# Kernel optimization log

Measured on AMD Instinct MI355X. Metric: run time of the kernel, lower is better.

## Reference

```python
import jax, jax.numpy as jnp
import numpy as np

N_DRUG, N_MICROBE = 1500, 1572
N = N_DRUG + N_MICROBE          # 3072 nodes
F_IN = 1546                     # raw feature dim (fc1: 1546 -> 256)
D0 = 256                        # GCN input dim after fc1
H1 = H2 = 128                   # GCN hidden dims (H1 + H2 = 256)
B = 16384                       # number of (left,right) query pairs


def _sym_norm(A):
    # D^{-1/2} A D^{-1/2} (no self loops), zeros kept for isolated nodes
    deg = A.sum(axis=1)
    d = jnp.where(deg > 0, jax.lax.rsqrt(deg), 0.0)
    return A * d[:, None] * d[None, :]


def _compute_inf(adj, L):
    # dl.compute_inf: L-hop influence = L-th power of sym-normalized adjacency
    An = _sym_norm(adj)
    M = An
    for _ in range(L - 1):
        M = M @ An
    return M


def _gcn_norm(W):
    # GCNConv normalization: add self loops (weight 1), sym-normalize by weighted degree
    Ahat = W + jnp.eye(W.shape[0], dtype=W.dtype)
    deg = Ahat.sum(axis=1)
    d = jnp.where(deg > 0, jax.lax.rsqrt(deg), 0.0)
    return Ahat * d[:, None] * d[None, :]


def _glorot(key, shape):
    return jax.random.normal(key, shape, dtype=jnp.float32) / np.sqrt(shape[0])


def setup_inputs() -> dict:
    key = jax.random.key(0)
    ks = jax.random.split(key, 24)
    u = jax.random.uniform(ks[0], (N, N), dtype=jnp.float32)
    w = jax.random.uniform(ks[1], (N, N), dtype=jnp.float32)
    adj = jnp.where(u < 0.01, w, 0.0)
    adj = jnp.maximum(adj, adj.T)
    X = jax.random.normal(ks[2], (N, F_IN), dtype=jnp.float32)
    left = jax.random.randint(ks[3], (B,), 0, N)
    right = jax.random.randint(ks[4], (B,), 0, N)
    return dict(
        left=left, right=right, X=X, adj=adj, threshold=jnp.float32(1e-4),
        W_fc1=_glorot(ks[5], (F_IN, D0)), b_fc1=jnp.zeros((D0,), jnp.float32),
        Wg1=_glorot(ks[6], (D0, H1)), bg1=jnp.zeros((H1,), jnp.float32),
        Wg2=_glorot(ks[7], (H1, H2)), bg2=jnp.zeros((H2,), jnp.float32),
        Wg3=_glorot(ks[8], (D0, H1)), bg3=jnp.zeros((H1,), jnp.float32),
        Wg4=_glorot(ks[9], (H1, H2)), bg4=jnp.zeros((H2,), jnp.float32),
        Wg5=_glorot(ks[10], (D0, H1)), bg5=jnp.zeros((H1,), jnp.float32),
        Wg6=_glorot(ks[11], (H1, H2)), bg6=jnp.zeros((H2,), jnp.float32),
        cnn_k=jax.random.normal(ks[12], (1, 3, 3, 3), dtype=jnp.float32) * 0.1,
        cnn_b=jnp.zeros((1,), jnp.float32),
        W_a=_glorot(ks[13], (2 * (H1 + H2), 64)), b_a=jnp.zeros((64,), jnp.float32),
        W_b=_glorot(ks[14], (64, 2)), b_b=jnp.zeros((2,), jnp.float32),
    )


def reference(left, right, X, adj, threshold,
              W_fc1, b_fc1, Wg1, bg1, Wg2, bg2, Wg3, bg3, Wg4, bg4,
              Wg5, bg5, Wg6, bg6, cnn_k, cnn_b, W_a, b_a, W_b, b_b):
    X0 = jax.nn.relu(X @ W_fc1 + b_fc1)  # fc1: [N, 1546] -> [N, 256]

    def branch(mask_src, Wa, ba, Wb, bb):
        # dynamically thresholded edges carry the ORIGINAL adj weights
        Wadj = jnp.where(mask_src > threshold, adj, 0.0)
        An = _gcn_norm(Wadj)                       # [N, N]
        e1 = jax.nn.relu(An @ (X0 @ Wa) + ba)      # GCNConv 1
        e2 = jax.nn.relu(An @ (e1 @ Wb) + bb)      # GCNConv 2
        return jnp.concatenate([e1, e2], axis=1)   # [N, 256]

    emb_l2 = branch(_compute_inf(adj, 2), Wg1, bg1, Wg2, bg2)
    emb_l1 = branch(_compute_inf(adj, 1), Wg3, bg3, Wg4, bg4)
    emb_l0 = branch(adj, Wg5, bg5, Wg6, bg6)

    emb = jnp.stack([emb_l0, emb_l1, emb_l2], axis=0)[None]  # [1, 3, N, 256]
    conv = jax.lax.conv_general_dilated(
        emb, cnn_k, window_strides=(1, 1), padding=[(2, 2), (2, 2)],
        rhs_dilation=(2, 2), dimension_numbers=('NCHW', 'OIHW', 'NCHW'))
    emb_all = conv[0, 0] + cnn_b[0]                # [N, 256]

    pair = jnp.concatenate([emb_all[left], emb_all[right]], axis=1)  # [B, 512]
    h = jax.nn.relu(pair @ W_a + b_a)              # dropout is identity at eval
    logits = h @ W_b + b_b                         # [B, 2]
    return logits, emb_all
```

## Files before the change

kernel.cpp:

```cpp
#include <hip/hip_runtime.h>

#define NN 3072
#define FIN 1546
#define KP 1568
#define MAXR 192
#define KSPLIT 7
#define KSLICE 224

#define XS4_BLOCKS (NN * KP / 1024)
#define WSPLIT_BLOCKS (256 * KP / 256)
#define WG_BLOCKS 704
#define CSR_BLOCKS (NN / 4)

typedef __attribute__((ext_vector_type(8))) __bf16 bf16x8;
typedef __attribute__((ext_vector_type(4))) __bf16 bf16x4;
typedef __attribute__((ext_vector_type(4))) float f32x4;

__global__ __launch_bounds__(256) void prep_k(const float* __restrict__ adj,
                                              int* __restrict__ cols, float* __restrict__ vals,
                                              int* __restrict__ cnt, float* __restrict__ dvec,
                                              const float* __restrict__ X,
                                              __bf16* __restrict__ Xh, __bf16* __restrict__ Xl,
                                              const float* __restrict__ W,
                                              __bf16* __restrict__ WhT, __bf16* __restrict__ WlT,
                                              const float* __restrict__ Wga0,
                                              const float* __restrict__ Wga1,
                                              const float* __restrict__ Wga2,
                                              const float* __restrict__ Wgb0,
                                              const float* __restrict__ Wgb1,
                                              const float* __restrict__ Wgb2,
                                              const float* __restrict__ Wa,
                                              __bf16* __restrict__ WgaTh, __bf16* __restrict__ WgaTl,
                                              __bf16* __restrict__ WgbTh, __bf16* __restrict__ WgbTl,
                                              __bf16* __restrict__ WaTh, __bf16* __restrict__ WaTl) {
    int bid = blockIdx.x;
    if (bid < XS4_BLOCKS) {
        int e = (bid * 256 + threadIdx.x) * 4;
        int i = e / KP, c = e - i * KP;
        const float* xr = X + (size_t)i * FIN + c;
        float x0 = (c + 0 < FIN) ? xr[0] : 0.f;
        float x1 = (c + 1 < FIN) ? xr[1] : 0.f;
        float x2 = (c + 2 < FIN) ? xr[2] : 0.f;
        float x3 = (c + 3 < FIN) ? xr[3] : 0.f;
        __bf16 h0 = (__bf16)x0, h1 = (__bf16)x1, h2 = (__bf16)x2, h3 = (__bf16)x3;
        bf16x4 hv = {h0, h1, h2, h3};
        bf16x4 lv = {(__bf16)(x0 - (float)h0), (__bf16)(x1 - (float)h1),
                     (__bf16)(x2 - (float)h2), (__bf16)(x3 - (float)h3)};
        *(bf16x4*)(Xh + e) = hv;
        *(bf16x4*)(Xl + e) = lv;
        return;
    }
    bid -= XS4_BLOCKS;
    if (bid < WSPLIT_BLOCKS) {
        int idx = bid * 256 + threadIdx.x;
        int c = idx / KP, k = idx - c * KP;
        float x = (k < FIN) ? W[(size_t)k * 256 + c] : 0.f;
        __bf16 h = (__bf16)x;
        WhT[idx] = h;
        WlT[idx] = (__bf16)(x - (float)h);
        return;
    }
    bid -= WSPLIT_BLOCKS;
    if (bid < WG_BLOCKS) {
        int idx = bid * 256 + threadIdx.x;
        float x;
        __bf16 *oh, *ol;
        int off;
        if (idx < 98304) {
            int b = idx >> 15, r = idx & 32767;
            int c = r >> 8, k = r & 255;
            const float* Wp = (b == 0) ? Wga0 : (b == 1) ? Wga1 : Wga2;
            x = Wp[k * 128 + c];
            oh = WgaTh; ol = WgaTl; off = idx;
        } else if (idx < 98304 + 49152) {
            int j = idx - 98304;
            int b = j >> 14, r = j & 16383;
            int c = r >> 7, k = r & 127;
            const float* Wp = (b == 0) ? Wgb0 : (b == 1) ? Wgb1 : Wgb2;
            x = Wp[k * 128 + c];
            oh = WgbTh; ol = WgbTl; off = j;
        } else {
            int j = idx - 147456;
            int c = j >> 8, k = j & 255;
            x = (c < 64) ? Wa[(size_t)k * 64 + c] : Wa[(size_t)(256 + k) * 64 + (c - 64)];
            oh = WaTh; ol = WaTl; off = j;
        }
        __bf16 h = (__bf16)x;
        oh[off] = h;
        ol[off] = (__bf16)(x - (float)h);
        return;
    }
    bid -= WG_BLOCKS;
    int i = bid * 4 + (threadIdx.x >> 6);
    int lane = threadIdx.x & 63;
    const float* row = adj + (size_t)i * NN;
    unsigned long long below = (1ull << lane) - 1ull;
    float s = 0.f; int count = 0;
    int base = i * MAXR;
    for (int c0 = 0; c0 < NN; c0 += 256) {
        float4 a4 = *(const float4*)(row + c0 + lane * 4);
        float a[4] = {a4.x, a4.y, a4.z, a4.w};
        s += a[0] + a[1] + a[2] + a[3];
        unsigned long long bal[4];
        #pragma unroll
        for (int u = 0; u < 4; u++) bal[u] = __ballot(a[u] != 0.f);
        int before = 0;
        #pragma unroll
        for (int u = 0; u < 4; u++) before += __popcll(bal[u] & below);
        int local = 0;
        #pragma unroll
        for (int u = 0; u < 4; u++) {
            if (a[u] != 0.f) {
                int pos = count + before + local;
                if (pos < MAXR) { cols[base + pos] = c0 + lane * 4 + u; vals[base + pos] = a[u]; }
                local++;
            }
        }
        int tot = 0;
        #pragma unroll
        for (int u = 0; u < 4; u++) tot += __popcll(bal[u]);
        count += tot;
    }
    for (int off = 32; off; off >>= 1) s += __shfl_xor(s, off);
    if (lane == 0) {
        cnt[i] = count < MAXR ? count : MAXR;
        dvec[i] = (s > 0.f) ? 1.0f / sqrtf(s) : 0.f;
    }
}

__global__ __launch_bounds__(256) void fc1m_k(const __bf16* __restrict__ Xh,
                                              const __bf16* __restrict__ Xl,
                                              const __bf16* __restrict__ WhT,
                                              const __bf16* __restrict__ WlT,
                                              float* __restrict__ Cpart) {
    int tid = threadIdx.x;
    int w = tid >> 6, lane = tid & 63;
    int m = lane & 15, q = lane >> 4;
    int i0 = blockIdx.x * 64, c0 = blockIdx.y * 64;
    int z = blockIdx.z;
    int k0 = z * KSLICE;
    int rowA = i0 + w * 16 + m;
    const __bf16* xh = Xh + (size_t)rowA * KP + k0 + q * 8;
    const __bf16* xl = Xl + (size_t)rowA * KP + k0 + q * 8;
    const __bf16* bh0 = WhT + (size_t)(c0 + m) * KP + k0 + q * 8;
    const __bf16* bl0 = WlT + (size_t)(c0 + m) * KP + k0 + q * 8;

    f32x4 acc[4];
    #pragma unroll
    for (int ct = 0; ct < 4; ct++)
        #pragma unroll
        for (int r = 0; r < 4; r++) acc[ct][r] = 0.f;

    for (int ks = 0; ks < KSLICE; ks += 32) {
        bf16x8 ah = *(const bf16x8*)(xh + ks);
        bf16x8 al = *(const bf16x8*)(xl + ks);
        #pragma unroll
        for (int ct = 0; ct < 4; ct++) {
            bf16x8 bh = *(const bf16x8*)(bh0 + (size_t)ct * 16 * KP + ks);
            bf16x8 bl = *(const bf16x8*)(bl0 + (size_t)ct * 16 * KP + ks);
            acc[ct] = __builtin_amdgcn_mfma_f32_16x16x32_bf16(ah, bh, acc[ct], 0, 0, 0);
            acc[ct] = __builtin_amdgcn_mfma_f32_16x16x32_bf16(ah, bl, acc[ct], 0, 0, 0);
            acc[ct] = __builtin_amdgcn_mfma_f32_16x16x32_bf16(al, bh, acc[ct], 0, 0, 0);
        }
    }
    float* outp = Cpart + (size_t)z * NN * 256;
    int rowBase = i0 + w * 16 + q * 4;
    #pragma unroll
    for (int ct = 0; ct < 4; ct++) {
        int col = c0 + ct * 16 + m;
        #pragma unroll
        for (int r = 0; r < 4; r++)
            outp[(size_t)(rowBase + r) * 256 + col] = acc[ct][r];
    }
}

__global__ __launch_bounds__(256) void maskall_k(const int* __restrict__ cols,
                                                 const float* __restrict__ vals,
                                                 const int* __restrict__ cnt,
                                                 const float* __restrict__ dvec,
                                                 const float* __restrict__ thrp,
                                                 int* __restrict__ mcols,
                                                 float* __restrict__ mvals,
                                                 int* __restrict__ mcnt,
                                                 float* __restrict__ db,
                                                 const float* __restrict__ Cpart,
                                                 const float* __restrict__ bias,
                                                 __bf16* __restrict__ X0h,
                                                 __bf16* __restrict__ X0l) {
    __shared__ float ds[NN];
    __shared__ int lcols[MAXR];
    __shared__ float lvals[MAXR];
    __shared__ int lcnt;
    __shared__ float osum;
    int i = blockIdx.x, tid = threadIdx.x, mode = blockIdx.y;

    if (mode == 3) {
        if (tid < 64) {
            int idx4 = i * 64 + tid;
            int c4 = tid << 2;
            float4 s = ((const float4*)Cpart)[idx4];
            #pragma unroll
            for (int z = 1; z < KSPLIT; z++) {
                float4 t = ((const float4*)(Cpart + (size_t)z * NN * 256))[idx4];
                s.x += t.x; s.y += t.y; s.z += t.z; s.w += t.w;
            }
            float4 b = *(const float4*)&bias[c4];
            s.x = fmaxf(s.x + b.x, 0.f); s.y = fmaxf(s.y + b.y, 0.f);
            s.z = fmaxf(s.z + b.z, 0.f); s.w = fmaxf(s.w + b.w, 0.f);
            __bf16 h0 = (__bf16)s.x, h1 = (__bf16)s.y, h2 = (__bf16)s.z, h3 = (__bf16)s.w;
            bf16x4 hv = {h0, h1, h2, h3};
            bf16x4 lv = {(__bf16)(s.x - (float)h0), (__bf16)(s.y - (float)h1),
                         (__bf16)(s.z - (float)h2), (__bf16)(s.w - (float)h3)};
            *(bf16x4*)(X0h + (size_t)i * 256 + c4) = hv;
            *(bf16x4*)(X0l + (size_t)i * 256 + c4) = lv;
        }
        return;
    }

    mcols += (size_t)mode * NN * MAXR;
    mvals += (size_t)mode * NN * MAXR;
    mcnt  += (size_t)mode * NN;
    db    += (size_t)mode * NN;
    int ni = cnt[i], base = i * MAXR;
    float thr = *thrp;
    float di = dvec[i];

    if (mode < 2) {
        if (tid == 0) lcnt = 0;
        __syncthreads();
        float s = 0.f;
        if (tid < ni) {
            int j = cols[base + tid];
            float a = vals[base + tid];
            float m = (mode == 0) ? a : a * di * dvec[j];
            if (m > thr) {
                int p = atomicAdd(&lcnt, 1);
                mcols[base + p] = j;
                mvals[base + p] = a;
                s = a;
            }
        }
        ds[tid] = s; __syncthreads();
        for (int off = 128; off; off >>= 1) {
            if (tid < off) ds[tid] += ds[tid + off];
            __syncthreads();
        }
        if (tid == 0) {
            mcnt[i] = lcnt;
            db[i] = 1.0f / sqrtf(ds[0] + 1.0f);
        }
        return;
    }

    if (tid == 0) { osum = 0.f; lcnt = 0; }
    for (int j = tid; j < NN; j += 256) ds[j] = 0.f;
    __syncthreads();
    for (int t = tid; t < ni; t += 256) {
        int j = cols[base + t];
        float a = vals[base + t];
        lcols[t] = j; lvals[t] = a;
        ds[j] = a * dvec[j] * dvec[j];
    }
    __syncthreads();
    int lane = tid & 63, wv = tid >> 6;
    int sub = lane & 15, dg = lane >> 4;
    for (int o = wv * 4 + dg; o < ni; o += 16) {
        int j = lcols[o];
        int nj = cnt[j], bj = j * MAXR;
        float dot = 0.f;
        for (int t = sub; t < nj; t += 16)
            dot += vals[bj + t] * ds[cols[bj + t]];
        #pragma unroll
        for (int off = 8; off; off >>= 1) dot += __shfl_xor(dot, off);
        if (sub == 0 && di * dvec[j] * dot > thr) {
            int p = atomicAdd(&lcnt, 1);
            mcols[base + p] = j;
            mvals[base + p] = lvals[o];
            atomicAdd(&osum, lvals[o]);
        }
    }
    __syncthreads();
    if (tid == 0) {
        mcnt[i] = lcnt;
        db[i] = 1.0f / sqrtf(osum + 1.0f);
    }
}

__global__ __launch_bounds__(256) void gemm3m_k(const __bf16* __restrict__ Ah,
                                                const __bf16* __restrict__ Al,
                                                int aplane, int K,
                                                const __bf16* __restrict__ Bh,
                                                const __bf16* __restrict__ Bl,
                                                float* __restrict__ out) {
    int tid = threadIdx.x;
    int w = tid >> 6, lane = tid & 63;
    int m = lane & 15, q = lane >> 4;
    int i0 = blockIdx.x * 64, c0 = blockIdx.y * 64;
    int z = blockIdx.z;
    int rowA = i0 + w * 16 + m;
    const __bf16* ah = Ah + (size_t)z * aplane + (size_t)rowA * K + q * 8;
    const __bf16* al = Al + (size_t)z * aplane + (size_t)rowA * K + q * 8;
    const __bf16* bh0 = Bh + (size_t)z * 128 * K + (size_t)(c0 + m) * K + q * 8;
    const __bf16* bl0 = Bl + (size_t)z * 128 * K + (size_t)(c0 + m) * K + q * 8;

    f32x4 acc[4];
    #pragma unroll
    for (int ct = 0; ct < 4; ct++)
        #pragma unroll
        for (int r = 0; r < 4; r++) acc[ct][r] = 0.f;

    for (int ks = 0; ks < K; ks += 32) {
        bf16x8 a_h = *(const bf16x8*)(ah + ks);
        bf16x8 a_l = *(const bf16x8*)(al + ks);
        #pragma unroll
        for (int ct = 0; ct < 4; ct++) {
            bf16x8 b_h = *(const bf16x8*)(bh0 + (size_t)ct * 16 * K + ks);
            bf16x8 b_l = *(const bf16x8*)(bl0 + (size_t)ct * 16 * K + ks);
            acc[ct] = __builtin_amdgcn_mfma_f32_16x16x32_bf16(a_h, b_h, acc[ct], 0, 0, 0);
            acc[ct] = __builtin_amdgcn_mfma_f32_16x16x32_bf16(a_h, b_l, acc[ct], 0, 0, 0);
            acc[ct] = __builtin_amdgcn_mfma_f32_16x16x32_bf16(a_l, b_h, acc[ct], 0, 0, 0);
        }
    }
    float* outp = out + (size_t)z * NN * 128;
    int rowBase = i0 + w * 16 + q * 4;
    #pragma unroll
    for (int ct = 0; ct < 4; ct++) {
        int col = c0 + ct * 16 + m;
        #pragma unroll
        for (int r = 0; r < 4; r++)
            outp[(size_t)(rowBase + r) * 128 + col] = acc[ct][r];
    }
}

__global__ __launch_bounds__(256) void spmm3_k(const int* __restrict__ mcols,
                                               const float* __restrict__ mvals,
                                               const int* __restrict__ mcnt,
                                               const float* __restrict__ db,
                                               const float* __restrict__ Xin,
                                               const float* __restrict__ bias0,
                                               const float* __restrict__ bias1,
                                               const float* __restrict__ bias2,
                                               __bf16* __restrict__ outAh,
                                               __bf16* __restrict__ outAl,
                                               float* __restrict__ embf, int coff) {
    __shared__ float lcoef[MAXR];
    __shared__ int lj[MAXR];
    __shared__ float4 part[8][32];
    int i = blockIdx.x, tid = threadIdx.x, b = blockIdx.y;
    mcols += (size_t)b * NN * MAXR;
    mvals += (size_t)b * NN * MAXR;
    mcnt  += (size_t)b * NN;
    db    += (size_t)b * NN;
    const float* Xb = Xin + (size_t)b * NN * 128;
    const float* bias = (b == 0) ? bias0 : (b == 1) ? bias1 : bias2;
    float dbi = db[i];
    int n = mcnt[i], base = i * MAXR;
    if (tid < n) {
        int j = mcols[base + tid];
        lj[tid] = j;
        lcoef[tid] = mvals[base + tid] * dbi * db[j];
    }
    __syncthreads();
    int g = tid >> 5, c4 = (tid & 31) << 2;
    float4 acc = make_float4(0.f, 0.f, 0.f, 0.f);
    float4 acc2 = make_float4(0.f, 0.f, 0.f, 0.f);
    if (g == 0) {
        float4 x = *(const float4*)&Xb[(size_t)i * 128 + c4];
        float d2 = dbi * dbi;
        acc = make_float4(d2 * x.x, d2 * x.y, d2 * x.z, d2 * x.w);
    }
    int t = g;
    for (; t + 8 < n; t += 16) {
        float cf0 = lcoef[t];
        float4 x0 = *(const float4*)&Xb[(size_t)lj[t] * 128 + c4];
        float cf1 = lcoef[t + 8];
        float4 x1 = *(const float4*)&Xb[(size_t)lj[t + 8] * 128 + c4];
        acc.x += cf0 * x0.x; acc.y += cf0 * x0.y; acc.z += cf0 * x0.z; acc.w += cf0 * x0.w;
        acc2.x += cf1 * x1.x; acc2.y += cf1 * x1.y; acc2.z += cf1 * x1.z; acc2.w += cf1 * x1.w;
    }
    if (t < n) {
        float cf = lcoef[t];
        float4 x = *(const float4*)&Xb[(size_t)lj[t] * 128 + c4];
        acc.x += cf * x.x; acc.y += cf * x.y; acc.z += cf * x.z; acc.w += cf * x.w;
    }
    acc.x += acc2.x; acc.y += acc2.y; acc.z += acc2.z; acc.w += acc2.w;
    part[g][tid & 31] = acc;
    __syncthreads();
    if (tid < 32) {
        float4 s = part[0][tid];
        #pragma unroll
        for (int gg = 1; gg < 8; gg++) {
            float4 t4 = part[gg][tid];
            s.x += t4.x; s.y += t4.y; s.z += t4.z; s.w += t4.w;
        }
        int cc = tid << 2;
        float4 bv = *(const float4*)&bias[cc];
        s.x = fmaxf(s.x + bv.x, 0.f); s.y = fmaxf(s.y + bv.y, 0.f);
        s.z = fmaxf(s.z + bv.z, 0.f); s.w = fmaxf(s.w + bv.w, 0.f);
        if (outAh) {
            __bf16 h0 = (__bf16)s.x, h1 = (__bf16)s.y, h2 = (__bf16)s.z, h3 = (__bf16)s.w;
            bf16x4 hv = {h0, h1, h2, h3};
            bf16x4 lv = {(__bf16)(s.x - (float)h0), (__bf16)(s.y - (float)h1),
                         (__bf16)(s.z - (float)h2), (__bf16)(s.w - (float)h3)};
            *(bf16x4*)(outAh + ((size_t)b * NN + i) * 128 + cc) = hv;
            *(bf16x4*)(outAl + ((size_t)b * NN + i) * 128 + cc) = lv;
        }
        *(float4*)&embf[((size_t)b * NN + i) * 256 + coff + cc] = s;
    }
}

__global__ __launch_bounds__(256) void conv3f_k(const float* __restrict__ emb,
                                                const float* __restrict__ ck,
                                                const float* __restrict__ cb,
                                                float* __restrict__ outf,
                                                __bf16* __restrict__ embh,
                                                __bf16* __restrict__ embl) {
    __shared__ float rows[3][3][256];
    int n = blockIdx.x, c = threadIdx.x;
    #pragma unroll
    for (int i = 0; i < 3; i++)
        #pragma unroll
        for (int kh = 0; kh < 3; kh++) {
            int nn2 = n + 2 * kh - 2;
            rows[i][kh][c] = (nn2 >= 0 && nn2 < NN) ? emb[((size_t)i * NN + nn2) * 256 + c] : 0.f;
        }
    __syncthreads();
    float s = cb[0];
    #pragma unroll
    for (int i = 0; i < 3; i++)
        #pragma unroll
        for (int kh = 0; kh < 3; kh++)
            #pragma unroll
            for (int kw = 0; kw < 3; kw++) {
                int cc = c + 2 * kw - 2;
                if (cc >= 0 && cc < 256)
                    s += rows[i][kh][cc] * ck[(i * 3 + kh) * 3 + kw];
            }
    size_t idx = (size_t)n * 256 + c;
    outf[idx] = s;
    __bf16 h = (__bf16)s;
    embh[idx] = h;
    embl[idx] = (__bf16)(s - (float)h);
}

__global__ __launch_bounds__(256) void gemmuvm_k(const __bf16* __restrict__ Ah,
                                                 const __bf16* __restrict__ Al,
                                                 const __bf16* __restrict__ Bh,
                                                 const __bf16* __restrict__ Bl,
                                                 float* __restrict__ uvp) {
    int tid = threadIdx.x;
    int w = tid >> 6, lane = tid & 63;
    int m = lane & 15, q = lane >> 4;
    int i0 = blockIdx.x * 64, c0 = blockIdx.y * 64;
    int z = blockIdx.z;
    int k0 = z * 128;
    int rowA = i0 + w * 16 + m;
    const __bf16* ah = Ah + (size_t)rowA * 256 + k0 + q * 8;
    const __bf16* al = Al + (size_t)rowA * 256 + k0 + q * 8;
    const __bf16* bh0 = Bh + (size_t)(c0 + m) * 256 + k0 + q * 8;
    const __bf16* bl0 = Bl + (size_t)(c0 + m) * 256 + k0 + q * 8;

    f32x4 acc[4];
    #pragma unroll
    for (int ct = 0; ct < 4; ct++)
        #pragma unroll
        for (int r = 0; r < 4; r++) acc[ct][r] = 0.f;

    for (int ks = 0; ks < 128; ks += 32) {
        bf16x8 a_h = *(const bf16x8*)(ah + ks);
        bf16x8 a_l = *(const bf16x8*)(al + ks);
        #pragma unroll
        for (int ct = 0; ct < 4; ct++) {
            bf16x8 b_h = *(const bf16x8*)(bh0 + (size_t)ct * 16 * 256 + ks);
            bf16x8 b_l = *(const bf16x8*)(bl0 + (size_t)ct * 16 * 256 + ks);
            acc[ct] = __builtin_amdgcn_mfma_f32_16x16x32_bf16(a_h, b_h, acc[ct], 0, 0, 0);
            acc[ct] = __builtin_amdgcn_mfma_f32_16x16x32_bf16(a_h, b_l, acc[ct], 0, 0, 0);
            acc[ct] = __builtin_amdgcn_mfma_f32_16x16x32_bf16(a_l, b_h, acc[ct], 0, 0, 0);
        }
    }
    float* outp = uvp + (size_t)z * NN * 128;
    int rowBase = i0 + w * 16 + q * 4;
    #pragma unroll
    for (int ct = 0; ct < 4; ct++) {
        int col = c0 + ct * 16 + m;
        #pragma unroll
        for (int r = 0; r < 4; r++)
            outp[(size_t)(rowBase + r) * 128 + col] = acc[ct][r];
    }
}

__global__ __launch_bounds__(256) void pairuv_k(const int* __restrict__ left,
                                                const int* __restrict__ right,
                                                const float* __restrict__ uvp,
                                                const float* __restrict__ ba,
                                                const float* __restrict__ Wb,
                                                const float* __restrict__ bb,
                                                float* __restrict__ out) {
    int tid = threadIdx.x;
    int w = tid >> 6, c = tid & 63;
    int base = blockIdx.x * 16 + w * 4;
    const float* u0 = uvp;
    const float* u1 = uvp + (size_t)NN * 128;
    float bac = ba[c];
    float w0 = Wb[c * 2], w1 = Wb[c * 2 + 1];
    float b0 = bb[0], b1 = bb[1];
    #pragma unroll
    for (int pp = 0; pp < 4; pp++) {
        int row = base + pp;
        int l = left[row], r = right[row];
        float h = u0[(size_t)l * 128 + c] + u1[(size_t)l * 128 + c]
                + u0[(size_t)r * 128 + 64 + c] + u1[(size_t)r * 128 + 64 + c] + bac;
        h = fmaxf(h, 0.f);
        float s0 = h * w0, s1 = h * w1;
        for (int off = 32; off; off >>= 1) {
            s0 += __shfl_xor(s0, off);
            s1 += __shfl_xor(s1, off);
        }
        if (c == 0) {
            out[row * 2]     = s0 + b0;
            out[row * 2 + 1] = s1 + b1;
        }
    }
}

extern "C" void kernel_launch(void* const* d_in, const int* in_sizes, int n_in,
                              void* d_out, int out_size, void* d_ws, size_t ws_size,
                              hipStream_t stream) {
    const int* left  = (const int*)d_in[0];
    const int* right = (const int*)d_in[1];
    const float* X    = (const float*)d_in[2];
    const float* adj  = (const float*)d_in[3];
    const float* thr  = (const float*)d_in[4];
    const float* Wfc1 = (const float*)d_in[5];
    const float* bfc1 = (const float*)d_in[6];
    const float* Wga[3] = { (const float*)d_in[15], (const float*)d_in[11], (const float*)d_in[7] };
    const float* bga[3] = { (const float*)d_in[16], (const float*)d_in[12], (const float*)d_in[8] };
    const float* Wgb[3] = { (const float*)d_in[17], (const float*)d_in[13], (const float*)d_in[9] };
    const float* bgb[3] = { (const float*)d_in[18], (const float*)d_in[14], (const float*)d_in[10] };
    const float* cnnk = (const float*)d_in[19];
    const float* cnnb = (const float*)d_in[20];
    const float* Wa_  = (const float*)d_in[21];
    const float* ba_  = (const float*)d_in[22];
    const float* Wb_  = (const float*)d_in[23];
    const float* bb_  = (const float*)d_in[24];

    char* p = (char*)d_ws;
    auto take = [&](size_t n) { char* q = p; p += (n + 255) & ~(size_t)255; return q; };
    float* dvec = (float*)take(NN * 4);
    float* db3  = (float*)take((size_t)3 * NN * 4);
    int*   cnt  = (int*)take(NN * 4);
    int*   mcnt3 = (int*)take((size_t)3 * NN * 4);
    int*   cols = (int*)take((size_t)NN * MAXR * 4);
    float* vals = (float*)take((size_t)NN * MAXR * 4);
    int*   mcols3 = (int*)take((size_t)3 * NN * MAXR * 4);
    float* mvals3 = (float*)take((size_t)3 * NN * MAXR * 4);
    __bf16* X0h  = (__bf16*)take((size_t)NN * 256 * 2);
    __bf16* X0l  = (__bf16*)take((size_t)NN * 256 * 2);
    float* XWall = (float*)take((size_t)3 * NN * 128 * 4);
    __bf16* e1h  = (__bf16*)take((size_t)3 * NN * 128 * 2);
    __bf16* e1l  = (__bf16*)take((size_t)3 * NN * 128 * 2);
    float* HW2all= (float*)take((size_t)3 * NN * 128 * 4);
    float* embf  = (float*)take((size_t)3 * NN * 256 * 4);
    __bf16* Xl   = (__bf16*)take((size_t)NN * KP * 2);
    __bf16* WhT  = (__bf16*)take((size_t)256 * KP * 2);
    __bf16* WlT  = (__bf16*)take((size_t)256 * KP * 2);
    __bf16* WgaTh = (__bf16*)take((size_t)3 * 128 * 256 * 2);
    __bf16* WgaTl = (__bf16*)take((size_t)3 * 128 * 256 * 2);
    __bf16* WgbTh = (__bf16*)take((size_t)3 * 128 * 128 * 2);
    __bf16* WgbTl = (__bf16*)take((size_t)3 * 128 * 128 * 2);
    __bf16* WaTh  = (__bf16*)take((size_t)128 * 256 * 2);
    __bf16* WaTl  = (__bf16*)take((size_t)128 * 256 * 2);
    __bf16* embh  = (__bf16*)take((size_t)NN * 256 * 2);
    __bf16* embl  = (__bf16*)take((size_t)NN * 256 * 2);
    __bf16* Xh = (__bf16*)mcols3;
    float* Cpart = XWall;
    float* uvp = embf;

    float* out_logits = (float*)d_out;
    float* out_emb = out_logits + 32768;

    prep_k<<<XS4_BLOCKS + WSPLIT_BLOCKS + WG_BLOCKS + CSR_BLOCKS, 256, 0, stream>>>(
        adj, cols, vals, cnt, dvec, X, Xh, Xl, Wfc1, WhT, WlT,
        Wga[0], Wga[1], Wga[2], Wgb[0], Wgb[1], Wgb[2], Wa_,
        WgaTh, WgaTl, WgbTh, WgbTl, WaTh, WaTl);

    fc1m_k<<<dim3(NN / 64, 4, KSPLIT), 256, 0, stream>>>(Xh, Xl, WhT, WlT, Cpart);

    maskall_k<<<dim3(NN, 4), 256, 0, stream>>>(cols, vals, cnt, dvec, thr,
                                               mcols3, mvals3, mcnt3, db3,
                                               Cpart, bfc1, X0h, X0l);

    gemm3m_k<<<dim3(NN / 64, 2, 3), 256, 0, stream>>>(X0h, X0l, 0, 256, WgaTh, WgaTl, XWall);
    spmm3_k<<<dim3(NN, 3), 256, 0, stream>>>(mcols3, mvals3, mcnt3, db3, XWall,
                                             bga[0], bga[1], bga[2], e1h, e1l, embf, 0);
    gemm3m_k<<<dim3(NN / 64, 2, 3), 256, 0, stream>>>(e1h, e1l, NN * 128, 128, WgbTh, WgbTl, HW2all);
    spmm3_k<<<dim3(NN, 3), 256, 0, stream>>>(mcols3, mvals3, mcnt3, db3, HW2all,
                                             bgb[0], bgb[1], bgb[2], (__bf16*)0, (__bf16*)0, embf, 128);

    conv3f_k<<<NN, 256, 0, stream>>>(embf, cnnk, cnnb, out_emb, embh, embl);
    gemmuvm_k<<<dim3(NN / 64, 2, 2), 256, 0, stream>>>(embh, embl, WaTh, WaTl, uvp);
    pairuv_k<<<16384 / 16, 256, 0, stream>>>(left, right, uvp, ba_, Wb_, bb_, out_logits);
}
```

Baseline: 307.9 us.

## Fuse fc1 GEMM into mask kernel and drop split-K partial buffers

Removes the split-K fc1 GEMM kernel and its partial-sum reduction. fc1 is now computed over the full K inside the mask kernel, running as extra blocks alongside the CSR masking work, with bias, relu and the bf16 hi/lo split fused into the epilogue. The uv GEMM also drops its K-split, so pairuv reads a single buffer. This saves a launch and the partial-sum traffic, but each fc1 block now loops over the full 1568-wide K with fewer blocks (192), so that part may become latency-bound. It also adds dedicated workspace for Xh and uvp.

Result: slower. 327.5 us (+6.4%).

```diff
diff --git a/kernel.cpp b/kernel.cpp
--- a/kernel.cpp
+++ b/kernel.cpp
@@ -4,13 +4,12 @@
 #define FIN 1546
 #define KP 1568
 #define MAXR 192
-#define KSPLIT 7
-#define KSLICE 224
 
 #define XS4_BLOCKS (NN * KP / 1024)
 #define WSPLIT_BLOCKS (256 * KP / 256)
 #define WG_BLOCKS 704
 #define CSR_BLOCKS (NN / 4)
+#define FC1_BLOCKS (NN / 16)
 
 typedef __attribute__((ext_vector_type(8))) __bf16 bf16x8;
 typedef __attribute__((ext_vector_type(4))) __bf16 bf16x4;
@@ -128,53 +127,7 @@
     }
 }
 
-__global__ __launch_bounds__(256) void fc1m_k(const __bf16* __restrict__ Xh,
-                                              const __bf16* __restrict__ Xl,
-                                              const __bf16* __restrict__ WhT,
-                                              const __bf16* __restrict__ WlT,
-                                              float* __restrict__ Cpart) {
-    int tid = threadIdx.x;
-    int w = tid >> 6, lane = tid & 63;
-    int m = lane & 15, q = lane >> 4;
-    int i0 = blockIdx.x * 64, c0 = blockIdx.y * 64;
-    int z = blockIdx.z;
-    int k0 = z * KSLICE;
-    int rowA = i0 + w * 16 + m;
-    const __bf16* xh = Xh + (size_t)rowA * KP + k0 + q * 8;
-    const __bf16* xl = Xl + (size_t)rowA * KP + k0 + q * 8;
-    const __bf16* bh0 = WhT + (size_t)(c0 + m) * KP + k0 + q * 8;
-    const __bf16* bl0 = WlT + (size_t)(c0 + m) * KP + k0 + q * 8;
-
-    f32x4 acc[4];
-    #pragma unroll
-    for (int ct = 0; ct < 4; ct++)
-        #pragma unroll
-        for (int r = 0; r < 4; r++) acc[ct][r] = 0.f;
-
-    for (int ks = 0; ks < KSLICE; ks += 32) {
-        bf16x8 ah = *(const bf16x8*)(xh + ks);
-        bf16x8 al = *(const bf16x8*)(xl + ks);
-        #pragma unroll
-        for (int ct = 0; ct < 4; ct++) {
-            bf16x8 bh = *(const bf16x8*)(bh0 + (size_t)ct * 16 * KP + ks);
-            bf16x8 bl = *(const bf16x8*)(bl0 + (size_t)ct * 16 * KP + ks);
-            acc[ct] = __builtin_amdgcn_mfma_f32_16x16x32_bf16(ah, bh, acc[ct], 0, 0, 0);
-            acc[ct] = __builtin_amdgcn_mfma_f32_16x16x32_bf16(ah, bl, acc[ct], 0, 0, 0);
-            acc[ct] = __builtin_amdgcn_mfma_f32_16x16x32_bf16(al, bh, acc[ct], 0, 0, 0);
-        }
-    }
-    float* outp = Cpart + (size_t)z * NN * 256;
-    int rowBase = i0 + w * 16 + q * 4;
-    #pragma unroll
-    for (int ct = 0; ct < 4; ct++) {
-        int col = c0 + ct * 16 + m;
-        #pragma unroll
-        for (int r = 0; r < 4; r++)
-            outp[(size_t)(rowBase + r) * 256 + col] = acc[ct][r];
-    }
-}
-
-__global__ __launch_bounds__(256) void maskall_k(const int* __restrict__ cols,
+__global__ __launch_bounds__(256) void fc1mask_k(const int* __restrict__ cols,
                                                  const float* __restrict__ vals,
                                                  const int* __restrict__ cnt,
                                                  const float* __restrict__ dvec,
@@ -183,7 +136,10 @@
                                                  float* __restrict__ mvals,
                                                  int* __restrict__ mcnt,
                                                  float* __restrict__ db,
-                                                 const float* __restrict__ Cpart,
+                                                 const __bf16* __restrict__ Xh,
+                                                 const __bf16* __restrict__ Xl,
+                                                 const __bf16* __restrict__ WhT,
+                                                 const __bf16* __restrict__ WlT,
                                                  const float* __restrict__ bias,
                                                  __bf16* __restrict__ X0h,
                                                  __bf16* __restrict__ X0l) {
@@ -192,30 +148,58 @@
     __shared__ float lvals[MAXR];
     __shared__ int lcnt;
     __shared__ float osum;
-    int i = blockIdx.x, tid = threadIdx.x, mode = blockIdx.y;
-
-    if (mode == 3) {
-        if (tid < 64) {
-            int idx4 = i * 64 + tid;
-            int c4 = tid << 2;
-            float4 s = ((const float4*)Cpart)[idx4];
+    int bid = blockIdx.x, tid = threadIdx.x;
+
+    if (bid < FC1_BLOCKS) {
+        int w = tid >> 6, lane = tid & 63;
+        int m = lane & 15, q = lane >> 4;
+        int r0 = bid * 16;
+        int rowA = r0 + m;
+        const __bf16* xh = Xh + (size_t)rowA * KP + q * 8;
+        const __bf16* xl = Xl + (size_t)rowA * KP + q * 8;
+        int c0 = w * 64;
+        const __bf16* bh0 = WhT + (size_t)(c0 + m) * KP + q * 8;
+        const __bf16* bl0 = WlT + (size_t)(c0 + m) * KP + q * 8;
+
+        f32x4 acc[4];
+        #pragma unroll
+        for (int ct = 0; ct < 4; ct++)
             #pragma unroll
-            for (int z = 1; z < KSPLIT; z++) {
-                float4 t = ((const float4*)(Cpart + (size_t)z * NN * 256))[idx4];
-                s.x += t.x; s.y += t.y; s.z += t.z; s.w += t.w;
+            for (int r = 0; r < 4; r++) acc[ct][r] = 0.f;
+
+        for (int ks = 0; ks < KP; ks += 32) {
+            bf16x8 ah = *(const bf16x8*)(xh + ks);
+            bf16x8 al = *(const bf16x8*)(xl + ks);
+            #pragma unroll
+            for (int ct = 0; ct < 4; ct++) {
+                bf16x8 bh = *(const bf16x8*)(bh0 + (size_t)ct * 16 * KP + ks);
+                bf16x8 bl = *(const bf16x8*)(bl0 + (size_t)ct * 16 * KP + ks);
+                acc[ct] = __builtin_amdgcn_mfma_f32_16x16x32_bf16(ah, bh, acc[ct], 0, 0, 0);
+                acc[ct] = __builtin_amdgcn_mfma_f32_16x16x32_bf16(ah, bl, acc[ct], 0, 0, 0);
+                acc[ct] = __builtin_amdgcn_mfma_f32_16x16x32_bf16(al, bh, acc[ct], 0, 0, 0);
             }
-            float4 b = *(const float4*)&bias[c4];
-            s.x = fmaxf(s.x + b.x, 0.f); s.y = fmaxf(s.y + b.y, 0.f);
-            s.z = fmaxf(s.z + b.z, 0.f); s.w = fmaxf(s.w + b.w, 0.f);
-            __bf16 h0 = (__bf16)s.x, h1 = (__bf16)s.y, h2 = (__bf16)s.z, h3 = (__bf16)s.w;
-            bf16x4 hv = {h0, h1, h2, h3};
-            bf16x4 lv = {(__bf16)(s.x - (float)h0), (__bf16)(s.y - (float)h1),
-                         (__bf16)(s.z - (float)h2), (__bf16)(s.w - (float)h3)};
-            *(bf16x4*)(X0h + (size_t)i * 256 + c4) = hv;
-            *(bf16x4*)(X0l + (size_t)i * 256 + c4) = lv;
+        }
+        #pragma unroll
+        for (int ct = 0; ct < 4; ct++) {
+            int col = c0 + ct * 16 + m;
+            float bv = bias[col];
+            #pragma unroll
+            for (int r = 0; r < 4; r++) {
+                int row = r0 + q * 4 + r;
+                float s = fmaxf(acc[ct][r] + bv, 0.f);
+                __bf16 h = (__bf16)s;
+                X0h[(size_t)row * 256 + col] = h;
+                X0l[(size_t)row * 256 + col] = (__bf16)(s - (float)h);
+            }
         }
         return;
     }
+
+    int t = bid - FC1_BLOCKS;
+    int mode, i;
+    if (t < NN)          { mode = 2; i = t; }
+    else if (t < 2 * NN) { mode = 0; i = t - NN; }
+    else                 { mode = 1; i = t - 2 * NN; }
 
     mcols += (size_t)mode * NN * MAXR;
     mvals += (size_t)mode * NN * MAXR;
@@ -255,10 +239,10 @@
     if (tid == 0) { osum = 0.f; lcnt = 0; }
     for (int j = tid; j < NN; j += 256) ds[j] = 0.f;
     __syncthreads();
-    for (int t = tid; t < ni; t += 256) {
-        int j = cols[base + t];
-        float a = vals[base + t];
-        lcols[t] = j; lvals[t] = a;
+    for (int t2 = tid; t2 < ni; t2 += 256) {
+        int j = cols[base + t2];
+        float a = vals[base + t2];
+        lcols[t2] = j; lvals[t2] = a;
         ds[j] = a * dvec[j] * dvec[j];
     }
     __syncthreads();
@@ -268,8 +252,8 @@
         int j = lcols[o];
         int nj = cnt[j], bj = j * MAXR;
         float dot = 0.f;
-        for (int t = sub; t < nj; t += 16)
-            dot += vals[bj + t] * ds[cols[bj + t]];
+        for (int t2 = sub; t2 < nj; t2 += 16)
+            dot += vals[bj + t2] * ds[cols[bj + t2]];
         #pragma unroll
         for (int off = 8; off; off >>= 1) dot += __shfl_xor(dot, off);
         if (sub == 0 && di * dvec[j] * dot > thr) {
@@ -452,13 +436,11 @@
     int w = tid >> 6, lane = tid & 63;
     int m = lane & 15, q = lane >> 4;
     int i0 = blockIdx.x * 64, c0 = blockIdx.y * 64;
-    int z = blockIdx.z;
-    int k0 = z * 128;
     int rowA = i0 + w * 16 + m;
-    const __bf16* ah = Ah + (size_t)rowA * 256 + k0 + q * 8;
-    const __bf16* al = Al + (size_t)rowA * 256 + k0 + q * 8;
-    const __bf16* bh0 = Bh + (size_t)(c0 + m) * 256 + k0 + q * 8;
-    const __bf16* bl0 = Bl + (size_t)(c0 + m) * 256 + k0 + q * 8;
+    const __bf16* ah = Ah + (size_t)rowA * 256 + q * 8;
+    const __bf16* al = Al + (size_t)rowA * 256 + q * 8;
+    const __bf16* bh0 = Bh + (size_t)(c0 + m) * 256 + q * 8;
+    const __bf16* bl0 = Bl + (size_t)(c0 + m) * 256 + q * 8;
 
     f32x4 acc[4];
     #pragma unroll
@@ -466,7 +448,7 @@
         #pragma unroll
         for (int r = 0; r < 4; r++) acc[ct][r] = 0.f;
 
-    for (int ks = 0; ks < 128; ks += 32) {
+    for (int ks = 0; ks < 256; ks += 32) {
         bf16x8 a_h = *(const bf16x8*)(ah + ks);
         bf16x8 a_l = *(const bf16x8*)(al + ks);
         #pragma unroll
@@ -478,14 +460,13 @@
             acc[ct] = __builtin_amdgcn_mfma_f32_16x16x32_bf16(a_l, b_h, acc[ct], 0, 0, 0);
         }
     }
-    float* outp = uvp + (size_t)z * NN * 128;
     int rowBase = i0 + w * 16 + q * 4;
     #pragma unroll
     for (int ct = 0; ct < 4; ct++) {
         int col = c0 + ct * 16 + m;
         #pragma unroll
         for (int r = 0; r < 4; r++)
-            outp[(size_t)(rowBase + r) * 128 + col] = acc[ct][r];
+            uvp[(size_t)(rowBase + r) * 128 + col] = acc[ct][r];
     }
 }
 
@@ -499,8 +480,6 @@
     int tid = threadIdx.x;
     int w = tid >> 6, c = tid & 63;
     int base = blockIdx.x * 16 + w * 4;
-    const float* u0 = uvp;
-    const float* u1 = uvp + (size_t)NN * 128;
     float bac = ba[c];
     float w0 = Wb[c * 2], w1 = Wb[c * 2 + 1];
     float b0 = bb[0], b1 = bb[1];
@@ -508,8 +487,7 @@
     for (int pp = 0; pp < 4; pp++) {
         int row = base + pp;
         int l = left[row], r = right[row];
-        float h = u0[(size_t)l * 128 + c] + u1[(size_t)l * 128 + c]
-                + u0[(size_t)r * 128 + 64 + c] + u1[(size_t)r * 128 + 64 + c] + bac;
+        float h = uvp[(size_t)l * 128 + c] + uvp[(size_t)r * 128 + 64 + c] + bac;
         h = fmaxf(h, 0.f);
         float s0 = h * w0, s1 = h * w1;
         for (int off = 32; off; off >>= 1) {
@@ -561,6 +539,7 @@
     __bf16* e1l  = (__bf16*)take((size_t)3 * NN * 128 * 2);
     float* HW2all= (float*)take((size_t)3 * NN * 128 * 4);
     float* embf  = (float*)take((size_t)3 * NN * 256 * 4);
+    __bf16* Xh   = (__bf16*)take((size_t)NN * KP * 2);
     __bf16* Xl   = (__bf16*)take((size_t)NN * KP * 2);
     __bf16* WhT  = (__bf16*)take((size_t)256 * KP * 2);
     __bf16* WlT  = (__bf16*)take((size_t)256 * KP * 2);
@@ -572,9 +551,7 @@
     __bf16* WaTl  = (__bf16*)take((size_t)128 * 256 * 2);
     __bf16* embh  = (__bf16*)take((size_t)NN * 256 * 2);
     __bf16* embl  = (__bf16*)take((size_t)NN * 256 * 2);
-    __bf16* Xh = (__bf16*)mcols3;
-    float* Cpart = XWall;
-    float* uvp = embf;
+    float* uvp   = (float*)take((size_t)NN * 128 * 4);
 
     float* out_logits = (float*)d_out;
     float* out_emb = out_logits + 32768;
@@ -584,11 +561,9 @@
         Wga[0], Wga[1], Wga[2], Wgb[0], Wgb[1], Wgb[2], Wa_,
         WgaTh, WgaTl, WgbTh, WgbTl, WaTh, WaTl);
 
-    fc1m_k<<<dim3(NN / 64, 4, KSPLIT), 256, 0, stream>>>(Xh, Xl, WhT, WlT, Cpart);
-
-    maskall_k<<<dim3(NN, 4), 256, 0, stream>>>(cols, vals, cnt, dvec, thr,
-                                               mcols3, mvals3, mcnt3, db3,
-                                               Cpart, bfc1, X0h, X0l);
+    fc1mask_k<<<FC1_BLOCKS + 3 * NN, 256, 0, stream>>>(cols, vals, cnt, dvec, thr,
+                                                       mcols3, mvals3, mcnt3, db3,
+                                                       Xh, Xl, WhT, WlT, bfc1, X0h, X0l);
 
     gemm3m_k<<<dim3(NN / 64, 2, 3), 256, 0, stream>>>(X0h, X0l, 0, 256, WgaTh, WgaTl, XWall);
     spmm3_k<<<dim3(NN, 3), 256, 0, stream>>>(mcols3, mvals3, mcnt3, db3, XWall,
@@ -598,6 +573,6 @@
                                              bgb[0], bgb[1], bgb[2], (__bf16*)0, (__bf16*)0, embf, 128);
 
     conv3f_k<<<NN, 256, 0, stream>>>(embf, cnnk, cnnb, out_emb, embh, embl);
-    gemmuvm_k<<<dim3(NN / 64, 2, 2), 256, 0, stream>>>(embh, embl, WaTh, WaTl, uvp);
+    gemmuvm_k<<<dim3(NN / 64, 2), 256, 0, stream>>>(embh, embl, WaTh, WaTl, uvp);
     pairuv_k<<<16384 / 16, 256, 0, stream>>>(left, right, uvp, ba_, Wb_, bb_, out_logits);
 }
```
